# Optimization experiments

Measured on AMD Instinct MI355X. Metric: run time of the kernel, lower is better.

## Reference

```python
import jax, jax.numpy as jnp
import numpy as np
import math


def _sinusoidal_pe(T, C, base=10000.0, dtype=jnp.float32):
    # Vaswani et al. interleaved sin/cos positional encoding, shape (T, C)
    position = jnp.arange(T, dtype=jnp.float32)[:, None]                      # (T,1)
    div_term = jnp.exp(jnp.arange(0, C, 2, dtype=jnp.float32) * (-math.log(base) / C))  # (C/2,)
    pe = jnp.zeros((T, C), dtype=jnp.float32)
    pe = pe.at[:, 0::2].set(jnp.sin(position * div_term))
    pe = pe.at[:, 1::2].set(jnp.cos(position * div_term))
    return pe.astype(dtype)


def setup_inputs() -> dict:
    key = jax.random.key(0)
    ks = jax.random.split(key, 7)
    B, T, C = 16, 8192, 1024
    s = 1.0 / math.sqrt(C)
    return {
        "x":   jax.random.normal(ks[0], (B, T, C), dtype=jnp.float32),
        "Wq":  jax.random.normal(ks[1], (C, C), dtype=jnp.float32) * s,
        "bq":  jax.random.normal(ks[2], (C,), dtype=jnp.float32) * s,
        "Wkv": jax.random.normal(ks[3], (C, 2 * C), dtype=jnp.float32) * s,
        "bkv": jax.random.normal(ks[4], (2 * C,), dtype=jnp.float32) * s,
        "Wo":  jax.random.normal(ks[5], (C, C), dtype=jnp.float32) * s,
        "bo":  jax.random.normal(ks[6], (C,), dtype=jnp.float32) * s,
    }


def reference(x, Wq, bq, Wkv, bkv, Wo, bo):
    B, T, C = x.shape
    H = 16
    D = C // H  # head_dim = 64

    # sinusoidal positional encoding (scale=False -> just add)
    x = x + _sinusoidal_pe(T, C, dtype=x.dtype)[None]

    # single-query projection (first token only) + full K/V projection
    q = x[:, :1, :] @ Wq + bq                       # (B, 1, C)
    kv = x @ Wkv + bkv                              # (B, T, 2C)
    k, v = kv[..., :C], kv[..., C:]                 # (B, T, C)

    # split heads
    q = q.reshape(B, 1, H, D).transpose(0, 2, 1, 3)  # (B, H, 1, D)
    k = k.reshape(B, T, H, D).transpose(0, 2, 1, 3)  # (B, H, T, D)
    v = v.reshape(B, T, H, D).transpose(0, 2, 1, 3)  # (B, H, T, D)

    # decode-style SDPA: one query vs T keys
    scale = 1.0 / math.sqrt(D)
    scores = jnp.einsum('bhqd,bhkd->bhqk', q, k) * scale   # (B, H, 1, T)
    attn = jax.nn.softmax(scores, axis=-1)
    y = jnp.einsum('bhqk,bhkd->bhqd', attn, v)             # (B, H, 1, D)

    # merge heads -> (B, C) and output projection
    y = y.transpose(0, 2, 1, 3).reshape(B, C)
    return y @ Wo + bo
```

## Files before the change

### kernel.cpp

```cpp
#include <hip/hip_runtime.h>
#include <math.h>

#define B 16
#define T 8192
#define C 1024
#define H 16
#define D 64

#define NCHUNK 32
#define CHUNK  256
#define RS     16
#define NST    (CHUNK/RS)

typedef unsigned short ushort_t;
typedef unsigned int uint_t;

typedef _Float16 half8  __attribute__((ext_vector_type(8)));
typedef _Float16 half4v __attribute__((ext_vector_type(4)));
typedef float    float4v __attribute__((ext_vector_type(4)));


__global__ void k_fdiv(double* __restrict__ fdiv) {
    int c = blockIdx.x * 256 + threadIdx.x;
    if (c < C) {
        int i2 = c & ~1;
        double e = exp((double)i2 * (-9.210340371976184 / 1024.0));
        fdiv[c] = e * 0.15915494309189535;
    }
}

__global__ void __launch_bounds__(256) k_q(const float* __restrict__ x,
                                           const float* __restrict__ Wq,
                                           const float* __restrict__ bq,
                                           float* __restrict__ q) {
    __shared__ float xs[C];
    __shared__ float red[4][64];
    int b = blockIdx.x >> 4;
    int cblk = blockIdx.x & 15;
    const float* xrow = x + (size_t)b * T * C;
    for (int i = threadIdx.x; i < C; i += 256)
        xs[i] = xrow[i] + ((i & 1) ? 1.0f : 0.0f);
    __syncthreads();
    int col = threadIdx.x & 63;
    int kg  = threadIdx.x >> 6;
    int c = cblk * 64 + col;
    float acc = 0.f;
#pragma unroll 8
    for (int k = kg * 256; k < kg * 256 + 256; ++k)
        acc += xs[k] * Wq[(size_t)k * C + c];
    red[kg][col] = acc;
    __syncthreads();
    if (kg == 0)
        q[b * C + c] = bq[c] + red[0][col] + red[1][col] + red[2][col] + red[3][col];
}

__global__ void __launch_bounds__(256) k_rt(const float* __restrict__ Wkv,
                                            const float* __restrict__ bkv,
                                            const float* __restrict__ q,
                                            float* __restrict__ rt,
                                            float* __restrict__ cc) {
    __shared__ float qs[D];
    int b = blockIdx.x >> 4, h = blockIdx.x & 15;
    if (threadIdx.x < D) qs[threadIdx.x] = q[b * C + h * D + threadIdx.x];
    __syncthreads();
    for (int c = threadIdx.x; c < C; c += 256) {
        const float4* wrow = (const float4*)(Wkv + (size_t)c * (2 * C) + h * D);
        float acc = 0.f;
#pragma unroll
        for (int d4 = 0; d4 < D / 4; ++d4) {
            float4 w = wrow[d4];
            acc += w.x * qs[d4 * 4 + 0] + w.y * qs[d4 * 4 + 1] +
                   w.z * qs[d4 * 4 + 2] + w.w * qs[d4 * 4 + 3];
        }
        rt[((size_t)b * C + c) * H + h] = acc * 0.125f;
    }
    if (threadIdx.x == 0) {
        float acc = 0.f;
        for (int d = 0; d < D; ++d) acc += bkv[h * D + d] * qs[d];
        cc[b * H + h] = acc * 0.125f;
    }
}

__global__ void __launch_bounds__(256, 2)
k_fused(const float* __restrict__ x,
        const float* __restrict__ rt,
        const float* __restrict__ cc,
        const double* __restrict__ fdiv,
        float* __restrict__ pacc,
        float* __restrict__ pl) {
    __shared__ _Float16 xa[RS * 1024];
    __shared__ float Sred[4 * RS * 16];
    __shared__ float p_lds[RS * 16];
    __shared__ float l_lds[16];
    __shared__ float cc_sh[16];

    const int tid = threadIdx.x;
    const int b  = blockIdx.x >> 5;
    const int t0 = (blockIdx.x & 31) * CHUNK;
    const int lane = tid & 63;
    const int wv   = tid >> 6;
    const int c0   = tid * 4;

    if (tid < 16) { cc_sh[tid] = cc[b * H + tid]; l_lds[tid] = 0.f; }

    const int m = lane & 15, g = lane >> 4;
    half8 rhf[8], rlf[8];
#pragma unroll
    for (int ks = 0; ks < 8; ++ks) {
#pragma unroll
        for (int j = 0; j < 8; ++j) {
            int c = wv * 256 + ks * 32 + g * 8 + j;
            float v = rt[((size_t)b * C + c) * H + m];
            _Float16 hi = (_Float16)v;
            rhf[ks][j] = hi;
            rlf[ks][j] = (_Float16)(v - (float)hi);
        }
    }

    const double fd0 = fdiv[c0];
    const double fd1 = fdiv[c0 + 2];

    const float* xbase = x + ((size_t)b * T + t0) * C + c0;

    float4v acc[16];
#pragma unroll
    for (int h = 0; h < 16; ++h) acc[h] = (float4v){0.f, 0.f, 0.f, 0.f};

    auto stage = [&](int st) {
        const float* xs = xbase + (size_t)st * RS * C;
#pragma unroll 4
        for (int r = 0; r < RS; ++r) {
            float4v xv = *(const float4v*)(xs + (size_t)r * C);
            double td = (double)(t0 + st * RS + r);
            double rev0 = td * fd0;
            double rev1 = td * fd1;
            float a0 = (float)(rev0 - floor(rev0)) * 6.283185307179586f;
            float a1 = (float)(rev1 - floor(rev1)) * 6.283185307179586f;
            float sn0, cs0, sn1, cs1;
            __sincosf(a0, &sn0, &cs0);
            __sincosf(a1, &sn1, &cs1);
            half4v hv;
            hv[0] = (_Float16)(xv[0] + sn0);
            hv[1] = (_Float16)(xv[1] + cs0);
            hv[2] = (_Float16)(xv[2] + sn1);
            hv[3] = (_Float16)(xv[3] + cs1);
            int elem = (r * 1024 + c0) ^ ((r & 7) << 3);
            *(half4v*)&xa[elem] = hv;
        }
    };

    stage(0);
    __syncthreads();

    for (int st = 0; st < NST; ++st) {
        float4v sac = {0.f, 0.f, 0.f, 0.f};
        const int abase = m * 1024 + wv * 256 + g * 8;
        const int aswz  = (m & 7) << 3;
#pragma unroll
        for (int ks = 0; ks < 8; ++ks) {
            half8 af = *(const half8*)&xa[(abase + ks * 32) ^ aswz];
            sac = __builtin_amdgcn_mfma_f32_16x16x32_f16(af, rhf[ks], sac, 0, 0, 0);
            sac = __builtin_amdgcn_mfma_f32_16x16x32_f16(af, rlf[ks], sac, 0, 0, 0);
        }
#pragma unroll
        for (int rg = 0; rg < 4; ++rg)
            Sred[wv * 256 + (g * 4 + rg) * 16 + m] = sac[rg];
        __syncthreads();

        {
            float s = Sred[tid] + Sred[256 + tid] + Sred[512 + tid] + Sred[768 + tid]
                    + cc_sh[tid & 15];
            p_lds[tid] = __expf(s);
        }
        __syncthreads();

        if (tid < 16) {
            float ls = 0.f;
#pragma unroll
            for (int r = 0; r < RS; ++r) ls += p_lds[r * 16 + tid];
            l_lds[tid] += ls;
        }
#pragma unroll 2
        for (int r = 0; r < RS; ++r) {
            int elem = (r * 1024 + c0) ^ ((r & 7) << 3);
            half4v xv = *(const half4v*)&xa[elem];
            float4v xvf = {(float)xv[0], (float)xv[1], (float)xv[2], (float)xv[3]};
            const float4v* pr = (const float4v*)&p_lds[r * 16];
            float4v p0 = pr[0], p1 = pr[1], p2 = pr[2], p3 = pr[3];
            float pvv[16] = {p0[0], p0[1], p0[2], p0[3],
                             p1[0], p1[1], p1[2], p1[3],
                             p2[0], p2[1], p2[2], p2[3],
                             p3[0], p3[1], p3[2], p3[3]};
#pragma unroll
            for (int h = 0; h < 16; ++h)
                acc[h] += xvf * pvv[h];
        }
        __syncthreads();
        if (st + 1 < NST) stage(st + 1);
        __syncthreads();
    }

    float* pb = pacc + (size_t)blockIdx.x * (H * C) + c0;
#pragma unroll
    for (int h = 0; h < 16; ++h)
        *(float4v*)&pb[h * 1024] = acc[h];
    if (tid < 16) pl[blockIdx.x * 16 + tid] = l_lds[tid];
}

__global__ void __launch_bounds__(256) k_combine(const float* __restrict__ pacc,
                                                 const float* __restrict__ pl,
                                                 float* __restrict__ sacc) {
    int b = blockIdx.x >> 4, h = blockIdx.x & 15;
    float l = 0.f;
#pragma unroll
    for (int ch = 0; ch < NCHUNK; ++ch)
        l += pl[((b << 5) + ch) * 16 + h];
    float inv = 1.0f / l;
    int c0 = threadIdx.x * 4;
    float4v s = {0.f, 0.f, 0.f, 0.f};
#pragma unroll 4
    for (int ch = 0; ch < NCHUNK; ++ch)
        s += *(const float4v*)&pacc[(((size_t)(b << 5) + ch) * 16 + h) * 1024 + c0];
    s *= inv;
    *(float4v*)&sacc[((size_t)(b * 16 + h)) * 1024 + c0] = s;
}

__global__ void __launch_bounds__(256) k_y(const float* __restrict__ Wkv,
                                           const float* __restrict__ bkv,
                                           const float* __restrict__ sacc,
                                           float* __restrict__ y) {
    __shared__ float sl[C];
    __shared__ float red[4][64];
    int b = blockIdx.x >> 4, h = blockIdx.x & 15;
    for (int i = threadIdx.x; i < C; i += 256)
        sl[i] = sacc[(size_t)(b * H + h) * C + i];
    __syncthreads();
    int col = threadIdx.x & 63;
    int kg  = threadIdx.x >> 6;
    int cy = h * 64 + col;
    float acc = 0.f;
#pragma unroll 8
    for (int c = kg * 256; c < kg * 256 + 256; ++c)
        acc += sl[c] * Wkv[(size_t)c * (2 * C) + C + cy];
    red[kg][col] = acc;
    __syncthreads();
    if (kg == 0)
        y[b * C + cy] = bkv[C + cy] + red[0][col] + red[1][col] + red[2][col] + red[3][col];
}

__global__ void __launch_bounds__(256) k_out(const float* __restrict__ Wo,
                                             const float* __restrict__ bo,
                                             const float* __restrict__ y,
                                             float* __restrict__ out) {
    __shared__ float yl[C];
    __shared__ float red[4][64];
    int b = blockIdx.x >> 4, jb = blockIdx.x & 15;
    for (int i = threadIdx.x; i < C; i += 256) yl[i] = y[b * C + i];
    __syncthreads();
    int col = threadIdx.x & 63;
    int kg  = threadIdx.x >> 6;
    int j = jb * 64 + col;
    float acc = 0.f;
#pragma unroll 8
    for (int k = kg * 256; k < kg * 256 + 256; ++k)
        acc += yl[k] * Wo[(size_t)k * C + j];
    red[kg][col] = acc;
    __syncthreads();
    if (kg == 0)
        out[b * C + j] = bo[j] + red[0][col] + red[1][col] + red[2][col] + red[3][col];
}

extern "C" void kernel_launch(void* const* d_in, const int* in_sizes, int n_in,
                              void* d_out, int out_size, void* d_ws, size_t ws_size,
                              hipStream_t stream) {
    const float* x   = (const float*)d_in[0];
    const float* Wq  = (const float*)d_in[1];
    const float* bq  = (const float*)d_in[2];
    const float* Wkv = (const float*)d_in[3];
    const float* bkv = (const float*)d_in[4];
    const float* Wo  = (const float*)d_in[5];
    const float* bo  = (const float*)d_in[6];
    float* out = (float*)d_out;

    char* w = (char*)d_ws;
    double* fdiv = (double*)w;
    float* q     = (float*)(w + 8192);
    float* rt    = q + (size_t)B * C;
    float* cc    = rt + (size_t)B * C * H;
    float* sacc  = cc + B * H;
    float* y     = sacc + (size_t)B * H * C;
    float* pacc  = y + B * C;
    float* pl    = pacc + (size_t)(B * NCHUNK) * H * C;

    k_fdiv<<<4, 256, 0, stream>>>(fdiv);
    k_q<<<B * 16, 256, 0, stream>>>(x, Wq, bq, q);
    k_rt<<<B * H, 256, 0, stream>>>(Wkv, bkv, q, rt, cc);
    k_fused<<<B * NCHUNK, 256, 0, stream>>>(x, rt, cc, fdiv, pacc, pl);
    k_combine<<<B * H, 256, 0, stream>>>(pacc, pl, sacc);
    k_y<<<B * 16, 256, 0, stream>>>(Wkv, bkv, sacc, y);
    k_out<<<B * 16, 256, 0, stream>>>(Wo, bo, y, out);
}
```

Baseline: 796.9 us.

## Double-buffer LDS staging in fused kernel and batch small GEMVs across batches

The fused attention kernel now uses two LDS buffers. It prefetches the next stage's x rows into registers before the MFMA score phase and writes the PE-added fp16 tile into the alternate buffer, which removes one barrier per stage and overlaps global loads with compute. The small q, rt, y and out kernels are restructured so each block handles four or sixteen batches, reusing each weight load across batches, and the combine kernel is folded into k_y. This raises register pressure from the 16-entry register prefetch at 2 blocks per SM and doubles LDS use, which could lower occupancy.

New measurement: 843.2 us. 5.8% more time.

```diff
diff --git a/kernel.cpp b/kernel.cpp
--- a/kernel.cpp
+++ b/kernel.cpp
@@ -33,25 +33,34 @@
                                            const float* __restrict__ Wq,
                                            const float* __restrict__ bq,
                                            float* __restrict__ q) {
-    __shared__ float xs[C];
-    __shared__ float red[4][64];
-    int b = blockIdx.x >> 4;
-    int cblk = blockIdx.x & 15;
-    const float* xrow = x + (size_t)b * T * C;
-    for (int i = threadIdx.x; i < C; i += 256)
-        xs[i] = xrow[i] + ((i & 1) ? 1.0f : 0.0f);
+    __shared__ float xst[C][4];
+    __shared__ float red[4][64][4];
+    int cblk = blockIdx.x >> 2, bg = blockIdx.x & 3;
+    for (int i = threadIdx.x; i < 4 * C; i += 256) {
+        int b4 = i >> 10, k = i & 1023;
+        xst[k][b4] = x[(size_t)(bg * 4 + b4) * T * C + k] + ((k & 1) ? 1.0f : 0.0f);
+    }
     __syncthreads();
     int col = threadIdx.x & 63;
     int kg  = threadIdx.x >> 6;
     int c = cblk * 64 + col;
-    float acc = 0.f;
-#pragma unroll 8
-    for (int k = kg * 256; k < kg * 256 + 256; ++k)
-        acc += xs[k] * Wq[(size_t)k * C + c];
-    red[kg][col] = acc;
-    __syncthreads();
-    if (kg == 0)
-        q[b * C + c] = bq[c] + red[0][col] + red[1][col] + red[2][col] + red[3][col];
+    float a[4] = {0.f, 0.f, 0.f, 0.f};
+#pragma unroll 4
+    for (int k = kg * 256; k < kg * 256 + 256; ++k) {
+        float w = Wq[(size_t)k * C + c];
+        float4v xv = *(const float4v*)&xst[k][0];
+#pragma unroll
+        for (int j = 0; j < 4; ++j) a[j] += xv[j] * w;
+    }
+#pragma unroll
+    for (int j = 0; j < 4; ++j) red[kg][col][j] = a[j];
+    __syncthreads();
+    if (kg == 0) {
+#pragma unroll
+        for (int j = 0; j < 4; ++j)
+            q[(size_t)(bg * 4 + j) * C + c] =
+                bq[c] + red[0][col][j] + red[1][col][j] + red[2][col][j] + red[3][col][j];
+    }
 }
 
 __global__ void __launch_bounds__(256) k_rt(const float* __restrict__ Wkv,
@@ -59,25 +68,35 @@
                                             const float* __restrict__ q,
                                             float* __restrict__ rt,
                                             float* __restrict__ cc) {
-    __shared__ float qs[D];
-    int b = blockIdx.x >> 4, h = blockIdx.x & 15;
-    if (threadIdx.x < D) qs[threadIdx.x] = q[b * C + h * D + threadIdx.x];
-    __syncthreads();
-    for (int c = threadIdx.x; c < C; c += 256) {
-        const float4* wrow = (const float4*)(Wkv + (size_t)c * (2 * C) + h * D);
-        float acc = 0.f;
-#pragma unroll
-        for (int d4 = 0; d4 < D / 4; ++d4) {
-            float4 w = wrow[d4];
-            acc += w.x * qs[d4 * 4 + 0] + w.y * qs[d4 * 4 + 1] +
-                   w.z * qs[d4 * 4 + 2] + w.w * qs[d4 * 4 + 3];
-        }
-        rt[((size_t)b * C + c) * H + h] = acc * 0.125f;
-    }
-    if (threadIdx.x == 0) {
-        float acc = 0.f;
-        for (int d = 0; d < D; ++d) acc += bkv[h * D + d] * qs[d];
-        cc[b * H + h] = acc * 0.125f;
+    __shared__ float qs[16][64];
+    int h = blockIdx.x >> 2, cq = blockIdx.x & 3;
+    for (int i = threadIdx.x; i < 16 * 64; i += 256) {
+        int b = i >> 6, d = i & 63;
+        qs[b][d] = q[(size_t)b * C + h * 64 + d];
+    }
+    __syncthreads();
+    int c = cq * 256 + threadIdx.x;
+    const float4* wrow = (const float4*)(Wkv + (size_t)c * (2 * C) + h * 64);
+    float acc[16];
+#pragma unroll
+    for (int b = 0; b < 16; ++b) acc[b] = 0.f;
+#pragma unroll
+    for (int d4 = 0; d4 < 16; ++d4) {
+        float4 w = wrow[d4];
+#pragma unroll
+        for (int b = 0; b < 16; ++b) {
+            const float4* q4 = (const float4*)&qs[b][d4 * 4];
+            acc[b] += w.x * q4->x + w.y * q4->y + w.z * q4->z + w.w * q4->w;
+        }
+    }
+#pragma unroll
+    for (int b = 0; b < 16; ++b)
+        rt[((size_t)b * C + c) * H + h] = acc[b] * 0.125f;
+    if (cq == 0 && threadIdx.x < 16) {
+        int b = threadIdx.x;
+        float a = 0.f;
+        for (int d = 0; d < 64; ++d) a += bkv[h * 64 + d] * qs[b][d];
+        cc[b * H + h] = a * 0.125f;
     }
 }
 
@@ -88,7 +107,7 @@
         const double* __restrict__ fdiv,
         float* __restrict__ pacc,
         float* __restrict__ pl) {
-    __shared__ _Float16 xa[RS * 1024];
+    __shared__ _Float16 xa[2][RS * 1024];
     __shared__ float Sred[4 * RS * 16];
     __shared__ float p_lds[RS * 16];
     __shared__ float l_lds[16];
@@ -119,18 +138,23 @@
 
     const double fd0 = fdiv[c0];
     const double fd1 = fdiv[c0 + 2];
-
     const float* xbase = x + ((size_t)b * T + t0) * C + c0;
 
     float4v acc[16];
 #pragma unroll
     for (int h = 0; h < 16; ++h) acc[h] = (float4v){0.f, 0.f, 0.f, 0.f};
 
-    auto stage = [&](int st) {
+    float4v xr[16];
+
+    auto loadregs = [&](int st) {
         const float* xs = xbase + (size_t)st * RS * C;
-#pragma unroll 4
+#pragma unroll
+        for (int r = 0; r < RS; ++r)
+            xr[r] = *(const float4v*)(xs + (size_t)r * C);
+    };
+    auto pewrite = [&](int st, int buf) {
+#pragma unroll
         for (int r = 0; r < RS; ++r) {
-            float4v xv = *(const float4v*)(xs + (size_t)r * C);
             double td = (double)(t0 + st * RS + r);
             double rev0 = td * fd0;
             double rev1 = td * fd1;
@@ -140,31 +164,37 @@
             __sincosf(a0, &sn0, &cs0);
             __sincosf(a1, &sn1, &cs1);
             half4v hv;
-            hv[0] = (_Float16)(xv[0] + sn0);
-            hv[1] = (_Float16)(xv[1] + cs0);
-            hv[2] = (_Float16)(xv[2] + sn1);
-            hv[3] = (_Float16)(xv[3] + cs1);
+            hv[0] = (_Float16)(xr[r][0] + sn0);
+            hv[1] = (_Float16)(xr[r][1] + cs0);
+            hv[2] = (_Float16)(xr[r][2] + sn1);
+            hv[3] = (_Float16)(xr[r][3] + cs1);
             int elem = (r * 1024 + c0) ^ ((r & 7) << 3);
-            *(half4v*)&xa[elem] = hv;
+            *(half4v*)&xa[buf][elem] = hv;
         }
     };
 
-    stage(0);
+    loadregs(0);
+    pewrite(0, 0);
     __syncthreads();
 
     for (int st = 0; st < NST; ++st) {
+        const int cur = st & 1;
+        if (st + 1 < NST) loadregs(st + 1);
+
         float4v sac = {0.f, 0.f, 0.f, 0.f};
         const int abase = m * 1024 + wv * 256 + g * 8;
         const int aswz  = (m & 7) << 3;
 #pragma unroll
         for (int ks = 0; ks < 8; ++ks) {
-            half8 af = *(const half8*)&xa[(abase + ks * 32) ^ aswz];
+            half8 af = *(const half8*)&xa[cur][(abase + ks * 32) ^ aswz];
             sac = __builtin_amdgcn_mfma_f32_16x16x32_f16(af, rhf[ks], sac, 0, 0, 0);
             sac = __builtin_amdgcn_mfma_f32_16x16x32_f16(af, rlf[ks], sac, 0, 0, 0);
         }
 #pragma unroll
         for (int rg = 0; rg < 4; ++rg)
             Sred[wv * 256 + (g * 4 + rg) * 16 + m] = sac[rg];
+
+        if (st + 1 < NST) pewrite(st + 1, cur ^ 1);
         __syncthreads();
 
         {
@@ -183,7 +213,7 @@
 #pragma unroll 2
         for (int r = 0; r < RS; ++r) {
             int elem = (r * 1024 + c0) ^ ((r & 7) << 3);
-            half4v xv = *(const half4v*)&xa[elem];
+            half4v xv = *(const half4v*)&xa[cur][elem];
             float4v xvf = {(float)xv[0], (float)xv[1], (float)xv[2], (float)xv[3]};
             const float4v* pr = (const float4v*)&p_lds[r * 16];
             float4v p0 = pr[0], p1 = pr[1], p2 = pr[2], p3 = pr[3];
@@ -196,8 +226,6 @@
                 acc[h] += xvf * pvv[h];
         }
         __syncthreads();
-        if (st + 1 < NST) stage(st + 1);
-        __syncthreads();
     }
 
     float* pb = pacc + (size_t)blockIdx.x * (H * C) + c0;
@@ -207,67 +235,89 @@
     if (tid < 16) pl[blockIdx.x * 16 + tid] = l_lds[tid];
 }
 
-__global__ void __launch_bounds__(256) k_combine(const float* __restrict__ pacc,
-                                                 const float* __restrict__ pl,
-                                                 float* __restrict__ sacc) {
-    int b = blockIdx.x >> 4, h = blockIdx.x & 15;
-    float l = 0.f;
-#pragma unroll
-    for (int ch = 0; ch < NCHUNK; ++ch)
-        l += pl[((b << 5) + ch) * 16 + h];
-    float inv = 1.0f / l;
-    int c0 = threadIdx.x * 4;
-    float4v s = {0.f, 0.f, 0.f, 0.f};
-#pragma unroll 4
-    for (int ch = 0; ch < NCHUNK; ++ch)
-        s += *(const float4v*)&pacc[(((size_t)(b << 5) + ch) * 16 + h) * 1024 + c0];
-    s *= inv;
-    *(float4v*)&sacc[((size_t)(b * 16 + h)) * 1024 + c0] = s;
-}
-
 __global__ void __launch_bounds__(256) k_y(const float* __restrict__ Wkv,
                                            const float* __restrict__ bkv,
-                                           const float* __restrict__ sacc,
+                                           const float* __restrict__ pacc,
+                                           const float* __restrict__ pl,
                                            float* __restrict__ y) {
-    __shared__ float sl[C];
-    __shared__ float red[4][64];
-    int b = blockIdx.x >> 4, h = blockIdx.x & 15;
-    for (int i = threadIdx.x; i < C; i += 256)
-        sl[i] = sacc[(size_t)(b * H + h) * C + i];
-    __syncthreads();
-    int col = threadIdx.x & 63;
-    int kg  = threadIdx.x >> 6;
+    __shared__ float st_[C][4];
+    __shared__ float red[4][64][4];
+    __shared__ float invl[4];
+    int h = blockIdx.x >> 2, bg = blockIdx.x & 3;
+    int c0 = threadIdx.x * 4;
+#pragma unroll
+    for (int b4 = 0; b4 < 4; ++b4) {
+        int b = bg * 4 + b4;
+        float4v s = {0.f, 0.f, 0.f, 0.f};
+#pragma unroll 4
+        for (int ch = 0; ch < NCHUNK; ++ch)
+            s += *(const float4v*)&pacc[(((size_t)b * NCHUNK + ch) * H + h) * 1024 + c0];
+        st_[c0 + 0][b4] = s[0];
+        st_[c0 + 1][b4] = s[1];
+        st_[c0 + 2][b4] = s[2];
+        st_[c0 + 3][b4] = s[3];
+    }
+    if (threadIdx.x < 4) {
+        int b = bg * 4 + threadIdx.x;
+        float l = 0.f;
+#pragma unroll
+        for (int ch = 0; ch < NCHUNK; ++ch) l += pl[(b * NCHUNK + ch) * H + h];
+        invl[threadIdx.x] = 1.0f / l;
+    }
+    __syncthreads();
+    int col = threadIdx.x & 63, kg = threadIdx.x >> 6;
     int cy = h * 64 + col;
-    float acc = 0.f;
-#pragma unroll 8
-    for (int c = kg * 256; c < kg * 256 + 256; ++c)
-        acc += sl[c] * Wkv[(size_t)c * (2 * C) + C + cy];
-    red[kg][col] = acc;
-    __syncthreads();
-    if (kg == 0)
-        y[b * C + cy] = bkv[C + cy] + red[0][col] + red[1][col] + red[2][col] + red[3][col];
+    float a[4] = {0.f, 0.f, 0.f, 0.f};
+#pragma unroll 4
+    for (int c = kg * 256; c < kg * 256 + 256; ++c) {
+        float w = Wkv[(size_t)c * (2 * C) + C + cy];
+        float4v sv = *(const float4v*)&st_[c][0];
+#pragma unroll
+        for (int j = 0; j < 4; ++j) a[j] += sv[j] * w;
+    }
+#pragma unroll
+    for (int j = 0; j < 4; ++j) red[kg][col][j] = a[j];
+    __syncthreads();
+    if (kg == 0) {
+#pragma unroll
+        for (int j = 0; j < 4; ++j)
+            y[(size_t)(bg * 4 + j) * C + cy] =
+                bkv[C + cy] +
+                (red[0][col][j] + red[1][col][j] + red[2][col][j] + red[3][col][j]) * invl[j];
+    }
 }
 
 __global__ void __launch_bounds__(256) k_out(const float* __restrict__ Wo,
                                              const float* __restrict__ bo,
                                              const float* __restrict__ y,
                                              float* __restrict__ out) {
-    __shared__ float yl[C];
-    __shared__ float red[4][64];
-    int b = blockIdx.x >> 4, jb = blockIdx.x & 15;
-    for (int i = threadIdx.x; i < C; i += 256) yl[i] = y[b * C + i];
-    __syncthreads();
-    int col = threadIdx.x & 63;
-    int kg  = threadIdx.x >> 6;
+    __shared__ float yt[C][4];
+    __shared__ float red[4][64][4];
+    int jb = blockIdx.x >> 2, bg = blockIdx.x & 3;
+    for (int i = threadIdx.x; i < 4 * C; i += 256) {
+        int b4 = i >> 10, k = i & 1023;
+        yt[k][b4] = y[(size_t)(bg * 4 + b4) * C + k];
+    }
+    __syncthreads();
+    int col = threadIdx.x & 63, kg = threadIdx.x >> 6;
     int j = jb * 64 + col;
-    float acc = 0.f;
-#pragma unroll 8
-    for (int k = kg * 256; k < kg * 256 + 256; ++k)
-        acc += yl[k] * Wo[(size_t)k * C + j];
-    red[kg][col] = acc;
-    __syncthreads();
-    if (kg == 0)
-        out[b * C + j] = bo[j] + red[0][col] + red[1][col] + red[2][col] + red[3][col];
+    float a[4] = {0.f, 0.f, 0.f, 0.f};
+#pragma unroll 4
+    for (int k = kg * 256; k < kg * 256 + 256; ++k) {
+        float w = Wo[(size_t)k * C + j];
+        float4v yv = *(const float4v*)&yt[k][0];
+#pragma unroll
+        for (int jj = 0; jj < 4; ++jj) a[jj] += yv[jj] * w;
+    }
+#pragma unroll
+    for (int jj = 0; jj < 4; ++jj) red[kg][col][jj] = a[jj];
+    __syncthreads();
+    if (kg == 0) {
+#pragma unroll
+        for (int jj = 0; jj < 4; ++jj)
+            out[(size_t)(bg * 4 + jj) * C + j] =
+                bo[j] + red[0][col][jj] + red[1][col][jj] + red[2][col][jj] + red[3][col][jj];
+    }
 }
 
 extern "C" void kernel_launch(void* const* d_in, const int* in_sizes, int n_in,
@@ -287,16 +337,14 @@
     float* q     = (float*)(w + 8192);
     float* rt    = q + (size_t)B * C;
     float* cc    = rt + (size_t)B * C * H;
-    float* sacc  = cc + B * H;
-    float* y     = sacc + (size_t)B * H * C;
+    float* y     = cc + B * H;
     float* pacc  = y + B * C;
     float* pl    = pacc + (size_t)(B * NCHUNK) * H * C;
 
     k_fdiv<<<4, 256, 0, stream>>>(fdiv);
-    k_q<<<B * 16, 256, 0, stream>>>(x, Wq, bq, q);
-    k_rt<<<B * H, 256, 0, stream>>>(Wkv, bkv, q, rt, cc);
+    k_q<<<64, 256, 0, stream>>>(x, Wq, bq, q);
+    k_rt<<<64, 256, 0, stream>>>(Wkv, bkv, q, rt, cc);
     k_fused<<<B * NCHUNK, 256, 0, stream>>>(x, rt, cc, fdiv, pacc, pl);
-    k_combine<<<B * H, 256, 0, stream>>>(pacc, pl, sacc);
-    k_y<<<B * 16, 256, 0, stream>>>(Wkv, bkv, sacc, y);
-    k_out<<<B * 16, 256, 0, stream>>>(Wo, bo, y, out);
-}
+    k_y<<<64, 256, 0, stream>>>(Wkv, bkv, pacc, pl, y);
+    k_out<<<64, 256, 0, stream>>>(Wo, bo, y, out);
+}
```
